# Kernel tuning notes

Hardware: AMD Instinct MI355X
Metric: run time of the kernel (lower is better)

## Reference

```python
import jax, jax.numpy as jnp
import numpy as np

HIDDEN = 2048
N_HEADS = 16
HEAD_DIM = HIDDEN // N_HEADS
ROPE_BASE = 10000.0


def rotate_half(x):
    half = x.shape[-1] // 2
    return jnp.concatenate((-x[..., half:], x[..., :half]), axis=-1)


def rope_cos_sin(seq_len, dtype):
    inv_freq = 1.0 / (ROPE_BASE ** (jnp.arange(0, HEAD_DIM, 2, dtype=jnp.float32) / HEAD_DIM))
    pos = jnp.arange(seq_len, dtype=jnp.float32)
    freqs = jnp.einsum('i,j->ij', pos, inv_freq)  # [S, hd/2]
    emb = jnp.concatenate((freqs, freqs), axis=-1)  # [S, hd]
    return jnp.cos(emb).astype(dtype), jnp.sin(emb).astype(dtype)


def setup_inputs() -> dict:
    key = jax.random.key(0)
    ks = jax.random.split(key, 9)
    B, S, H = 2, 2048, HIDDEN
    std = 1.0 / np.sqrt(H)
    return {
        'hidden_states': jax.random.normal(ks[0], (B, S, H), dtype=jnp.float32),
        'Wq': jax.random.uniform(ks[1], (H, H), jnp.float32, -std, std),
        'bq': jax.random.uniform(ks[2], (H,), jnp.float32, -std, std),
        'Wk': jax.random.uniform(ks[3], (H, H), jnp.float32, -std, std),
        'bk': jax.random.uniform(ks[4], (H,), jnp.float32, -std, std),
        'Wv': jax.random.uniform(ks[5], (H, H), jnp.float32, -std, std),
        'bv': jax.random.uniform(ks[6], (H,), jnp.float32, -std, std),
        'Wo': jax.random.uniform(ks[7], (H, H), jnp.float32, -std, std),
        'bo': jax.random.uniform(ks[8], (H,), jnp.float32, -std, std),
    }


def reference(hidden_states, Wq, bq, Wk, bk, Wv, bv, Wo, bo):
    B, S, H = hidden_states.shape
    scale = HEAD_DIM ** -0.5

    def proj(W, b):
        # torch Linear: x @ W.T + b
        y = jnp.einsum('bsh,oh->bso', hidden_states, W) + b
        return y.reshape(B, S, N_HEADS, HEAD_DIM).transpose(0, 2, 1, 3)  # [B,nh,S,hd]

    q = proj(Wq, bq)
    k = proj(Wk, bk)
    v = proj(Wv, bv)

    cos, sin = rope_cos_sin(S, hidden_states.dtype)  # [S, hd]
    cos = cos[None, None, :, :]
    sin = sin[None, None, :, :]
    q = q * cos + rotate_half(q) * sin
    k = k * cos + rotate_half(k) * sin

    scores = jnp.einsum('bhqd,bhkd->bhqk', q, k) * scale  # [B,nh,S,S]
    probs = jax.nn.softmax(scores, axis=-1)
    ctx = jnp.einsum('bhqk,bhkd->bhqd', probs, v)
    ctx = ctx.transpose(0, 2, 1, 3).reshape(B, S, H)
    return jnp.einsum('bsh,oh->bso', ctx, Wo) + bo
```

## Files before the change

kernel.cpp:

```cpp
#include <hip/hip_runtime.h>
#include <hip/hip_bf16.h>
#include <math.h>

#define HIDDEN 2048
#define NH 16
#define HD 128
#define NB 2
#define SEQ 2048
#define K_DIM 2048

typedef unsigned int u32;
typedef unsigned short ushort_t;
typedef __bf16 bf16x8 __attribute__((ext_vector_type(8)));
typedef float f32x4 __attribute__((ext_vector_type(4)));
typedef ushort_t u16x8 __attribute__((ext_vector_type(8)));

__device__ __forceinline__ void split1(float x, unsigned short& h, unsigned short& l) {
    u32 u = __float_as_uint(x);
    u32 hr = (u + 0x7FFFu + ((u >> 16) & 1u)) >> 16;
    h = (unsigned short)hr;
    float r = x - __uint_as_float(hr << 16);
    u32 u2 = __float_as_uint(r);
    l = (unsigned short)((u2 + 0x7FFFu + ((u2 >> 16) & 1u)) >> 16);
}

__device__ __forceinline__ ushort_t bf16r(float x) {
    u32 u = __float_as_uint(x);
    return (ushort_t)((u + 0x7FFFu + ((u >> 16) & 1u)) >> 16);
}

__device__ __forceinline__ void gl_lds16(const void* g, void* l) {
    __builtin_amdgcn_global_load_lds(
        (const __attribute__((address_space(1))) u32*)g,
        (__attribute__((address_space(3))) u32*)l, 16, 0, 0);
}

__global__ void k_rope_tables(float* __restrict__ ct, float* __restrict__ st) {
    int idx = blockIdx.x * 256 + threadIdx.x;
    int s = idx >> 6, d = idx & 63;
    double inv = pow(10000.0, -(double)d * (1.0 / 64.0));
    double ang = (double)s * inv;
    ct[idx] = (float)cos(ang);
    st[idx] = (float)sin(ang);
}

#define XG 2097152
#define WG 1048576
__global__ void k_cvt_all(const float4* __restrict__ X, const float4* __restrict__ W0,
                          const float4* __restrict__ W1, const float4* __restrict__ W2,
                          ushort4* __restrict__ Xh, ushort4* __restrict__ H0,
                          ushort4* __restrict__ H1, ushort4* __restrict__ H2) {
    int idx = blockIdx.x * 256 + threadIdx.x;
    const float4* src;
    ushort4* dst;
    int off;
    if (idx < XG) { src = X; dst = Xh; off = idx; }
    else {
        int t = idx - XG;
        int m = t >> 20;
        off = t & (WG - 1);
        src = (m == 0) ? W0 : (m == 1) ? W1 : W2;
        dst = (m == 0) ? H0 : (m == 1) ? H1 : H2;
    }
    float4 x = src[off];
    ushort4 h;
    h.x = bf16r(x.x); h.y = bf16r(x.y); h.z = bf16r(x.z); h.w = bf16r(x.w);
    dst[off] = h;
}

__global__ void k_split(const float4* __restrict__ src, ushort4* __restrict__ hi,
                        ushort4* __restrict__ lo) {
    int idx = blockIdx.x * 256 + threadIdx.x;
    float4 x = src[idx];
    ushort4 h, l;
    split1(x.x, h.x, l.x);
    split1(x.y, h.y, l.y);
    split1(x.z, h.z, l.z);
    split1(x.w, h.w, l.w);
    hi[idx] = h;
    lo[idx] = l;
}

__global__ __launch_bounds__(256)
void k_gemm_qkv(const ushort_t* __restrict__ Xh,
                const ushort_t* __restrict__ W0, const ushort_t* __restrict__ W1,
                const ushort_t* __restrict__ W2,
                const float* __restrict__ b0, const float* __restrict__ b1,
                const float* __restrict__ b2,
                float* __restrict__ o0, float* __restrict__ o1, float* __restrict__ o2) {
    __shared__ ushort_t As[128 * 32];
    __shared__ ushort_t Bs[128 * 32];
    const int tid = threadIdx.x;
    const int lane = tid & 63;
    const int w = tid >> 6;
    const int wm = w & 1, wn = w >> 1;
    const int quad = lane >> 4;
    const int l15 = lane & 15;
    const int m0 = blockIdx.x << 7;
    const int mat = blockIdx.y >> 4;
    const int n0 = (blockIdx.y & 15) << 7;
    const ushort_t* Wsel = (mat == 0) ? W0 : (mat == 1) ? W1 : W2;
    const float* bias = (mat == 0) ? b0 : (mat == 1) ? b1 : b2;
    float* out = (mat == 0) ? o0 : (mat == 1) ? o1 : o2;

    const ushort_t* src = (w < 2) ? Xh : Wsel;
    const int rbase = ((w < 2) ? m0 : n0) + (w & 1) * 64;
    ushort_t* lbase = ((w < 2) ? As : Bs) + (w & 1) * 64 * 32;
    const int lrow = lane >> 2;
    const int lk = (lane & 3) << 3;
    const ushort_t* gp[4];
    ushort_t* lp[4];
#pragma unroll
    for (int i = 0; i < 4; i++) {
        gp[i] = src + (size_t)(rbase + i * 16 + lrow) * K_DIM + lk;
        lp[i] = lbase + i * 512;
    }

    f32x4 acc[4][4];
#pragma unroll
    for (int i = 0; i < 4; i++)
#pragma unroll
        for (int j = 0; j < 4; j++) acc[i][j] = (f32x4){0.f, 0.f, 0.f, 0.f};

    const int aoff = (wm * 64 + l15) * 32 + quad * 8;
    const int boff = (wn * 64 + l15) * 32 + quad * 8;

#pragma unroll
    for (int i = 0; i < 4; i++) gl_lds16(gp[i], lp[i]);
    __syncthreads();
    bf16x8 ah[4], bh[4];
#pragma unroll
    for (int f = 0; f < 4; f++) {
        ah[f] = *(const bf16x8*)&As[aoff + f * 512];
        bh[f] = *(const bf16x8*)&Bs[boff + f * 512];
    }

    for (int kt = 32; kt <= K_DIM; kt += 32) {
        __syncthreads();
        if (kt < K_DIM) {
#pragma unroll
            for (int i = 0; i < 4; i++) gl_lds16(gp[i] + kt, lp[i]);
        }
#pragma unroll
        for (int fm = 0; fm < 4; fm++)
#pragma unroll
            for (int fn = 0; fn < 4; fn++)
                acc[fm][fn] = __builtin_amdgcn_mfma_f32_16x16x32_bf16(ah[fm], bh[fn], acc[fm][fn], 0, 0, 0);
        if (kt < K_DIM) {
            __syncthreads();
#pragma unroll
            for (int f = 0; f < 4; f++) {
                ah[f] = *(const bf16x8*)&As[aoff + f * 512];
                bh[f] = *(const bf16x8*)&Bs[boff + f * 512];
            }
        }
    }

    float bcolv[4];
#pragma unroll
    for (int fn = 0; fn < 4; fn++) bcolv[fn] = bias[n0 + wn * 64 + fn * 16 + l15];

    const int h = n0 >> 7;
    const int bb = m0 >> 11;
    const int sb = (m0 & (SEQ - 1)) + wm * 64 + quad * 4;
    const int d = wn * 64 + l15;
    float* obase = out + ((size_t)(bb * NH + h) * SEQ) * HD;
#pragma unroll
    for (int fm = 0; fm < 4; fm++)
#pragma unroll
        for (int fn = 0; fn < 4; fn++)
#pragma unroll
            for (int r = 0; r < 4; r++)
                obase[(size_t)(sb + fm * 16 + r) * HD + d + fn * 16] =
                    acc[fm][fn][r] + bcolv[fn];
}

__global__ __launch_bounds__(256)
void k_gemm_o(const ushort_t* __restrict__ Ah, const ushort_t* __restrict__ Al,
              const ushort_t* __restrict__ Bh, const ushort_t* __restrict__ Bl,
              const float* __restrict__ bias, float* __restrict__ out) {
    __shared__ ushort_t lds[4][128 * 32];
    const int tid = threadIdx.x;
    const int lane = tid & 63;
    const int w = tid >> 6;
    const int wm = w & 1, wn = w >> 1;
    const int quad = lane >> 4;
    const int l15 = lane & 15;
    const int m0 = blockIdx.x << 7;
    const int n0 = blockIdx.y << 7;
    const bool isA = (w < 2);

    const ushort_t* src = (w == 0) ? Ah : (w == 1) ? Al : (w == 2) ? Bh : Bl;
    const int lrow = lane >> 2;
    const int lk = (lane & 3) << 3;
    const ushort_t* gp[8];
    ushort_t* lp[8];
#pragma unroll
    for (int i = 0; i < 8; i++) {
        if (isA) {
            int m = m0 + i * 16 + lrow;
            int bb = m >> 11, s = m & (SEQ - 1);
            gp[i] = src + ((size_t)bb * NH * SEQ + s) * HD + lk;
        } else {
            gp[i] = src + (size_t)(n0 + i * 16 + lrow) * K_DIM + lk;
        }
        lp[i] = &lds[w][i * 512];
    }

    f32x4 acc[4][4];
#pragma unroll
    for (int i = 0; i < 4; i++)
#pragma unroll
        for (int j = 0; j < 4; j++) acc[i][j] = (f32x4){0.f, 0.f, 0.f, 0.f};

    const int aoff = (wm * 64 + l15) * 32 + quad * 8;
    const int boff = (wn * 64 + l15) * 32 + quad * 8;

#pragma unroll
    for (int i = 0; i < 8; i++) gl_lds16(gp[i], lp[i]);
    __syncthreads();
    bf16x8 ah[4], al[4], bh[4], bl[4];
#pragma unroll
    for (int f = 0; f < 4; f++) {
        ah[f] = *(const bf16x8*)&lds[0][aoff + f * 512];
        al[f] = *(const bf16x8*)&lds[1][aoff + f * 512];
        bh[f] = *(const bf16x8*)&lds[2][boff + f * 512];
        bl[f] = *(const bf16x8*)&lds[3][boff + f * 512];
    }

    for (int kt = 32; kt <= K_DIM; kt += 32) {
        __syncthreads();
        if (kt < K_DIM) {
            const size_t koff = isA ? ((size_t)(kt >> 7) * (SEQ * HD) + (kt & 127)) : (size_t)kt;
#pragma unroll
            for (int i = 0; i < 8; i++) gl_lds16(gp[i] + koff, lp[i]);
        }
#pragma unroll
        for (int fm = 0; fm < 4; fm++)
#pragma unroll
            for (int fn = 0; fn < 4; fn++) {
                acc[fm][fn] = __builtin_amdgcn_mfma_f32_16x16x32_bf16(ah[fm], bh[fn], acc[fm][fn], 0, 0, 0);
                acc[fm][fn] = __builtin_amdgcn_mfma_f32_16x16x32_bf16(ah[fm], bl[fn], acc[fm][fn], 0, 0, 0);
                acc[fm][fn] = __builtin_amdgcn_mfma_f32_16x16x32_bf16(al[fm], bh[fn], acc[fm][fn], 0, 0, 0);
            }
        if (kt < K_DIM) {
            __syncthreads();
#pragma unroll
            for (int f = 0; f < 4; f++) {
                ah[f] = *(const bf16x8*)&lds[0][aoff + f * 512];
                al[f] = *(const bf16x8*)&lds[1][aoff + f * 512];
                bh[f] = *(const bf16x8*)&lds[2][boff + f * 512];
                bl[f] = *(const bf16x8*)&lds[3][boff + f * 512];
            }
        }
    }

    float bcolv[4];
#pragma unroll
    for (int fn = 0; fn < 4; fn++) bcolv[fn] = bias[n0 + wn * 64 + fn * 16 + l15];

    const int mb = m0 + wm * 64 + quad * 4;
    const int nb = n0 + wn * 64 + l15;
#pragma unroll
    for (int fm = 0; fm < 4; fm++)
#pragma unroll
        for (int fn = 0; fn < 4; fn++)
#pragma unroll
            for (int r = 0; r < 4; r++)
                out[(size_t)(mb + fm * 16 + r) * HIDDEN + nb + fn * 16] =
                    acc[fm][fn][r] + bcolv[fn];
}

__global__ void k_rope_pack(const float* __restrict__ q, const float* __restrict__ k,
                            const float* __restrict__ ct, const float* __restrict__ st,
                            ushort_t* __restrict__ Qb, ushort_t* __restrict__ Kb) {
    int idx = blockIdx.x * 256 + threadIdx.x;
    int d = idx & 63;
    int s = (idx >> 6) & (SEQ - 1);
    int bh = idx >> 17;
    size_t base = ((size_t)bh * SEQ + s) * HD;
    float c = ct[(s << 6) + d], sn = st[(s << 6) + d];
    const float scq = 0.08838834764831845f;
    float q0 = q[base + d], q1 = q[base + d + 64];
    Qb[base + d]      = bf16r((q0 * c - q1 * sn) * scq);
    Qb[base + d + 64] = bf16r((q1 * c + q0 * sn) * scq);
    float k0 = k[base + d], k1 = k[base + d + 64];
    Kb[base + d]      = bf16r(k0 * c - k1 * sn);
    Kb[base + d + 64] = bf16r(k1 * c + k0 * sn);
}

__global__ __launch_bounds__(256)
void k_vpack(const float* __restrict__ v, ushort_t* __restrict__ vt) {
    __shared__ float t[64][65];
    const int tid = threadIdx.x;
    const int bh = blockIdx.z;
    const int s0 = blockIdx.x << 6;
    const int d0 = blockIdx.y << 6;
    const float* src = v + ((size_t)bh * SEQ + s0) * HD + d0;
    const int rr = tid >> 4;
    const int cc = (tid & 15) << 2;
#pragma unroll
    for (int i = 0; i < 4; i++) {
        float4 x = *(const float4*)(src + (size_t)(i * 16 + rr) * HD + cc);
        t[i * 16 + rr][cc] = x.x;
        t[i * 16 + rr][cc + 1] = x.y;
        t[i * 16 + rr][cc + 2] = x.z;
        t[i * 16 + rr][cc + 3] = x.w;
    }
    __syncthreads();
    const int dr = tid >> 2;
    const int sc_ = (tid & 3) << 4;
    ushort_t* dst = vt + ((size_t)bh * HD + d0 + dr) * SEQ + s0 + sc_;
    u16x8 o0, o1;
#pragma unroll
    for (int u = 0; u < 8; u++) o0[u] = bf16r(t[sc_ + u][dr]);
#pragma unroll
    for (int u = 0; u < 8; u++) o1[u] = bf16r(t[sc_ + 8 + u][dr]);
    *(u16x8*)dst = o0;
    *(u16x8*)(dst + 8) = o1;
}

__global__ __launch_bounds__(256, 2)
void k_flash_mfma(const ushort_t* __restrict__ Qb, const ushort_t* __restrict__ Kb,
                  const ushort_t* __restrict__ Vt,
                  ushort_t* __restrict__ ch, ushort_t* __restrict__ cl) {
    __shared__ ushort_t KV[128 * 136];
    __shared__ ushort_t Ps[128 * 136];
    const int tid = threadIdx.x;
    const int lane = tid & 63;
    const int w = tid >> 6;
    const int quad = lane >> 4;
    const int l15 = lane & 15;
    const int bi = blockIdx.x;
    const int bh = bi & 31;
    const int qt = bi >> 5;
    const ushort_t* Qg = Qb + ((size_t)bh * SEQ + ((size_t)qt << 7)) * HD;
    const ushort_t* Kg = Kb + (size_t)bh * SEQ * HD;
    const ushort_t* Vg = Vt + (size_t)bh * HD * SEQ;

    bf16x8 qf[2][4];
#pragma unroll
    for (int qi = 0; qi < 2; qi++)
#pragma unroll
        for (int ks = 0; ks < 4; ks++)
            qf[qi][ks] = *(const bf16x8*)(Qg + (size_t)(w * 32 + qi * 16 + l15) * HD + ks * 32 + quad * 8);

    const int sr = tid >> 4;
    const int sc8 = (tid & 15) << 3;

    u16x8 Kreg[8], Vreg[8];
#pragma unroll
    for (int i = 0; i < 8; i++)
        Kreg[i] = *(const u16x8*)(Kg + (size_t)(i * 16 + sr) * HD + sc8);
#pragma unroll
    for (int i = 0; i < 8; i++)
        Vreg[i] = *(const u16x8*)(Vg + (size_t)(i * 16 + sr) * SEQ + sc8);

    f32x4 acc[2][8];
#pragma unroll
    for (int qi = 0; qi < 2; qi++)
#pragma unroll
        for (int d = 0; d < 8; d++) acc[qi][d] = (f32x4){0.f, 0.f, 0.f, 0.f};
    float lp[2] = {0.f, 0.f};

    for (int kt = 0; kt < SEQ; kt += 128) {
        const int np = kt + 128;
        __syncthreads();
#pragma unroll
        for (int i = 0; i < 8; i++)
            *(u16x8*)&KV[(i * 16 + sr) * 136 + sc8] = Kreg[i];
        if (np < SEQ) {
#pragma unroll
            for (int i = 0; i < 8; i++)
                Kreg[i] = *(const u16x8*)(Kg + (size_t)(np + i * 16 + sr) * HD + sc8);
        }
        __syncthreads();

        f32x4 sc[2][8];
#pragma unroll
        for (int qi = 0; qi < 2; qi++)
#pragma unroll
            for (int j = 0; j < 8; j++) sc[qi][j] = (f32x4){0.f, 0.f, 0.f, 0.f};
#pragma unroll
        for (int ks = 0; ks < 4; ks++) {
#pragma unroll
            for (int jh = 0; jh < 2; jh++) {
                bf16x8 kf[4];
#pragma unroll
                for (int j = 0; j < 4; j++)
                    kf[j] = *(const bf16x8*)&KV[((jh * 4 + j) * 16 + l15) * 136 + ks * 32 + quad * 8];
#pragma unroll
                for (int qi = 0; qi < 2; qi++)
#pragma unroll
                    for (int j = 0; j < 4; j++)
                        sc[qi][jh * 4 + j] = __builtin_amdgcn_mfma_f32_16x16x32_bf16(
                            kf[j], qf[qi][ks], sc[qi][jh * 4 + j], 0, 0, 0);
            }
        }

#pragma unroll
        for (int qi = 0; qi < 2; qi++) {
            const int prow = (w * 32 + qi * 16 + l15) * 136 + quad * 4;
#pragma unroll
            for (int j = 0; j < 8; j++) {
                float p0 = __expf(sc[qi][j][0]);
                float p1 = __expf(sc[qi][j][1]);
                float p2 = __expf(sc[qi][j][2]);
                float p3 = __expf(sc[qi][j][3]);
                lp[qi] += (p0 + p1) + (p2 + p3);
                __hip_bfloat162 lo2 = __float22bfloat162_rn({p0, p1});
                __hip_bfloat162 hi2 = __float22bfloat162_rn({p2, p3});
                uint2 pk = make_uint2(*(u32*)&lo2, *(u32*)&hi2);
                *(uint2*)&Ps[prow + j * 16] = pk;
            }
        }
        __syncthreads();
#pragma unroll
        for (int i = 0; i < 8; i++)
            *(u16x8*)&KV[(i * 16 + sr) * 136 + sc8] = Vreg[i];
        if (np < SEQ) {
#pragma unroll
            for (int i = 0; i < 8; i++)
                Vreg[i] = *(const u16x8*)(Vg + (size_t)(i * 16 + sr) * SEQ + np + sc8);
        }
        __syncthreads();

#pragma unroll
        for (int ks = 0; ks < 4; ks++) {
            bf16x8 pf[2];
#pragma unroll
            for (int qi = 0; qi < 2; qi++)
                pf[qi] = *(const bf16x8*)&Ps[(w * 32 + qi * 16 + l15) * 136 + ks * 32 + quad * 8];
#pragma unroll
            for (int db = 0; db < 8; db++) {
                bf16x8 vf = *(const bf16x8*)&KV[(db * 16 + l15) * 136 + ks * 32 + quad * 8];
#pragma unroll
                for (int qi = 0; qi < 2; qi++)
                    acc[qi][db] = __builtin_amdgcn_mfma_f32_16x16x32_bf16(vf, pf[qi], acc[qi][db], 0, 0, 0);
            }
        }
    }

    float inv[2];
#pragma unroll
    for (int qi = 0; qi < 2; qi++) {
        float l = lp[qi];
        l += __shfl_xor(l, 16);
        l += __shfl_xor(l, 32);
        inv[qi] = 1.0f / l;
    }
    const size_t obase = ((size_t)bh * SEQ + ((size_t)qt << 7)) * HD;

    __syncthreads();
#pragma unroll
    for (int qi = 0; qi < 2; qi++)
#pragma unroll
        for (int db = 0; db < 8; db++) {
            ushort4 hh;
            ushort_t dum;
            split1(acc[qi][db][0] * inv[qi], hh.x, dum);
            split1(acc[qi][db][1] * inv[qi], hh.y, dum);
            split1(acc[qi][db][2] * inv[qi], hh.z, dum);
            split1(acc[qi][db][3] * inv[qi], hh.w, dum);
            *(ushort4*)&Ps[(w * 32 + qi * 16 + l15) * 136 + db * 16 + quad * 4] = hh;
        }
    __syncthreads();
#pragma unroll
    for (int t = 0; t < 8; t++) {
        int c = t * 256 + tid;
        int row = c >> 4, col8 = (c & 15) << 3;
        *(u16x8*)&ch[obase + (size_t)row * HD + col8] = *(const u16x8*)&Ps[row * 136 + col8];
    }
    __syncthreads();
#pragma unroll
    for (int qi = 0; qi < 2; qi++)
#pragma unroll
        for (int db = 0; db < 8; db++) {
            ushort4 ll;
            ushort_t dum;
            split1(acc[qi][db][0] * inv[qi], dum, ll.x);
            split1(acc[qi][db][1] * inv[qi], dum, ll.y);
            split1(acc[qi][db][2] * inv[qi], dum, ll.z);
            split1(acc[qi][db][3] * inv[qi], dum, ll.w);
            *(ushort4*)&Ps[(w * 32 + qi * 16 + l15) * 136 + db * 16 + quad * 4] = ll;
        }
    __syncthreads();
#pragma unroll
    for (int t = 0; t < 8; t++) {
        int c = t * 256 + tid;
        int row = c >> 4, col8 = (c & 15) << 3;
        *(u16x8*)&cl[obase + (size_t)row * HD + col8] = *(const u16x8*)&Ps[row * 136 + col8];
    }
}

extern "C" void kernel_launch(void* const* d_in, const int* in_sizes, int n_in,
                              void* d_out, int out_size, void* d_ws, size_t ws_size,
                              hipStream_t stream) {
    const float* X  = (const float*)d_in[0];
    const float* Wq = (const float*)d_in[1];
    const float* bq = (const float*)d_in[2];
    const float* Wk = (const float*)d_in[3];
    const float* bk = (const float*)d_in[4];
    const float* Wv = (const float*)d_in[5];
    const float* bv = (const float*)d_in[6];
    const float* Wo = (const float*)d_in[7];
    const float* bo = (const float*)d_in[8];
    float* out = (float*)d_out;

    const size_t QS = (size_t)NB * NH * SEQ * HD;
    const size_t WS = (size_t)HIDDEN * HIDDEN;
    float* q_ws = (float*)d_ws;
    float* k_ws = q_ws + QS;
    float* v_ws = k_ws + QS;
    float* cost = v_ws + QS;
    float* sint = cost + (size_t)SEQ * 64;
    ushort_t* Xh = (ushort_t*)(sint + (size_t)SEQ * 64);
    ushort_t* Wh0 = Xh + QS;
    ushort_t* Wh1 = Wh0 + WS;
    ushort_t* Wh2 = Wh1 + WS;
    ushort_t* Woh = Wh2 + WS;
    ushort_t* Wol = Woh + WS;
    ushort_t* Kb  = Wol + WS;
    ushort_t* Vtb = Kb + QS;
    ushort_t* ctxh = (ushort_t*)q_ws;
    ushort_t* ctxl = ctxh + QS;

    k_rope_tables<<<(SEQ * 64) / 256, 256, 0, stream>>>(cost, sint);

    k_cvt_all<<<(XG + 3 * WG) / 256, 256, 0, stream>>>(
        (const float4*)X, (const float4*)Wq, (const float4*)Wk, (const float4*)Wv,
        (ushort4*)Xh, (ushort4*)Wh0, (ushort4*)Wh1, (ushort4*)Wh2);
    k_split<<<WS / 4 / 256, 256, 0, stream>>>((const float4*)Wo, (ushort4*)Woh, (ushort4*)Wol);

    k_gemm_qkv<<<dim3(32, 48), 256, 0, stream>>>(Xh, Wh0, Wh1, Wh2, bq, bk, bv,
                                                 q_ws, k_ws, v_ws);

    ushort_t* Qbb = Xh;
    k_rope_pack<<<(NB * NH * SEQ * 64) / 256, 256, 0, stream>>>(q_ws, k_ws, cost, sint, Qbb, Kb);
    k_vpack<<<dim3(SEQ / 64, HD / 64, NB * NH), 256, 0, stream>>>(v_ws, Vtb);

    k_flash_mfma<<<512, 256, 0, stream>>>(Qbb, Kb, Vtb, ctxh, ctxl);

    k_gemm_o<<<dim3(32, 16), 256, 0, stream>>>(ctxh, ctxl, Woh, Wol, bo, out);
}
```

Before: 500.8 us.

## Rewrite QKV GEMM as 256x256-tile 8-wave kernel with double-buffered swizzled LDS

Replaces the 128x128, 4-wave QKV projection GEMM with a 256x256-tile, 512-thread kernel that uses a K-step of 64 and double-buffered LDS. The main loop is interleaved into phases so global-to-LDS loads overlap MFMA work, with explicit waitcnt, barriers and s_setprio. LDS columns are XOR-swizzled to reduce bank conflicts, and block IDs are remapped for better L2 locality. The larger tile raises data reuse per block, at the cost of only 384 blocks and heavy register and LDS use (128 KB), which may limit occupancy.

```diff
diff --git a/kernel.cpp b/kernel.cpp
--- a/kernel.cpp
+++ b/kernel.cpp
@@ -81,98 +81,158 @@
     lo[idx] = l;
 }
 
-__global__ __launch_bounds__(256)
-void k_gemm_qkv(const ushort_t* __restrict__ Xh,
-                const ushort_t* __restrict__ W0, const ushort_t* __restrict__ W1,
-                const ushort_t* __restrict__ W2,
-                const float* __restrict__ b0, const float* __restrict__ b1,
-                const float* __restrict__ b2,
-                float* __restrict__ o0, float* __restrict__ o1, float* __restrict__ o2) {
-    __shared__ ushort_t As[128 * 32];
-    __shared__ ushort_t Bs[128 * 32];
+#define BAR  __builtin_amdgcn_s_barrier()
+#define LGKM0 asm volatile("s_waitcnt lgkmcnt(0)" ::: "memory")
+#define VM4  asm volatile("s_waitcnt vmcnt(4)" ::: "memory")
+#define VM0  asm volatile("s_waitcnt vmcnt(0)" ::: "memory")
+#define PRIO1 __builtin_amdgcn_s_setprio(1)
+#define PRIO0 __builtin_amdgcn_s_setprio(0)
+
+#define STA(slot, half, kt) do { \
+    const ushort_t* g_ = Xh + sgA + (size_t)((half) * 128) * 2048 + (size_t)(kt) * 64; \
+    gl_lds16(g_, &As[slot][((half) * 128 + w * 16) * 64]); \
+    gl_lds16(g_ + 8 * 2048, &As[slot][((half) * 128 + w * 16 + 8) * 64]); \
+} while (0)
+
+#define STB(slot, half, kt) do { \
+    const ushort_t* g_ = Wsel + sgB + (size_t)((half) * 128) * 2048 + (size_t)(kt) * 64; \
+    gl_lds16(g_, &Bs[slot][((half) * 128 + w * 16) * 64]); \
+    gl_lds16(g_ + 8 * 2048, &Bs[slot][((half) * 128 + w * 16 + 8) * 64]); \
+} while (0)
+
+#define RD_A4(DST, slot, MB) \
+    _Pragma("unroll") for (int mf = 0; mf < 4; mf++) { \
+        DST[mf][0] = *(const bf16x8*)&As[slot][arow + ((MB) + mf) * 1024 + cc0]; \
+        DST[mf][1] = *(const bf16x8*)&As[slot][arow + ((MB) + mf) * 1024 + cc1]; \
+    }
+
+#define RD_B2(DST, slot, NBB) \
+    _Pragma("unroll") for (int nf = 0; nf < 2; nf++) { \
+        DST[nf][0] = *(const bf16x8*)&Bs[slot][brow + ((NBB) + nf) * 1024 + cc0]; \
+        DST[nf][1] = *(const bf16x8*)&Bs[slot][brow + ((NBB) + nf) * 1024 + cc1]; \
+    }
+
+#define PH_MFMA(AF, BF, MB, NBB) do { PRIO1; \
+    _Pragma("unroll") for (int mf = 0; mf < 4; mf++) \
+    _Pragma("unroll") for (int nf = 0; nf < 2; nf++) { \
+        acc[(MB) + mf][(NBB) + nf] = __builtin_amdgcn_mfma_f32_16x16x32_bf16( \
+            AF[mf][0], BF[nf][0], acc[(MB) + mf][(NBB) + nf], 0, 0, 0); \
+        acc[(MB) + mf][(NBB) + nf] = __builtin_amdgcn_mfma_f32_16x16x32_bf16( \
+            AF[mf][1], BF[nf][1], acc[(MB) + mf][(NBB) + nf], 0, 0, 0); \
+    } PRIO0; } while (0)
+
+__global__ __launch_bounds__(512, 2)
+void k_gemm_qkv8(const ushort_t* __restrict__ Xh,
+                 const ushort_t* __restrict__ W0, const ushort_t* __restrict__ W1,
+                 const ushort_t* __restrict__ W2,
+                 const float* __restrict__ b0, const float* __restrict__ b1,
+                 const float* __restrict__ b2,
+                 float* __restrict__ o0, float* __restrict__ o1, float* __restrict__ o2) {
+    __shared__ ushort_t As[2][256 * 64];
+    __shared__ ushort_t Bs[2][256 * 64];
     const int tid = threadIdx.x;
     const int lane = tid & 63;
     const int w = tid >> 6;
-    const int wm = w & 1, wn = w >> 1;
+    const int wm = w >> 2;
+    const int wn = w & 3;
     const int quad = lane >> 4;
     const int l15 = lane & 15;
-    const int m0 = blockIdx.x << 7;
-    const int mat = blockIdx.y >> 4;
-    const int n0 = (blockIdx.y & 15) << 7;
+
+    int bid = blockIdx.x;
+    bid = (bid & 7) * 48 + (bid >> 3);
+    const int bx = bid & 15;
+    const int by = bid >> 4;
+    const int m0 = bx << 8;
+    const int mat = by >> 3;
+    const int n0 = (by & 7) << 8;
     const ushort_t* Wsel = (mat == 0) ? W0 : (mat == 1) ? W1 : W2;
     const float* bias = (mat == 0) ? b0 : (mat == 1) ? b1 : b2;
     float* out = (mat == 0) ? o0 : (mat == 1) ? o1 : o2;
 
-    const ushort_t* src = (w < 2) ? Xh : Wsel;
-    const int rbase = ((w < 2) ? m0 : n0) + (w & 1) * 64;
-    ushort_t* lbase = ((w < 2) ? As : Bs) + (w & 1) * 64 * 32;
-    const int lrow = lane >> 2;
-    const int lk = (lane & 3) << 3;
-    const ushort_t* gp[4];
-    ushort_t* lp[4];
-#pragma unroll
-    for (int i = 0; i < 4; i++) {
-        gp[i] = src + (size_t)(rbase + i * 16 + lrow) * K_DIM + lk;
-        lp[i] = lbase + i * 512;
-    }
-
-    f32x4 acc[4][4];
-#pragma unroll
-    for (int i = 0; i < 4; i++)
+    const int lrow = lane >> 3;
+    const int lcol8 = (((lane & 7) ^ lrow) << 3);
+    const size_t sgA = (size_t)(m0 + w * 16 + lrow) * 2048 + lcol8;
+    const size_t sgB = (size_t)(n0 + w * 16 + lrow) * 2048 + lcol8;
+
+    const int arow = (wm * 128 + l15) * 64;
+    const int brow = (wn * 64 + l15) * 64;
+    const int cc0 = ((quad ^ (l15 & 7)) << 3);
+    const int cc1 = cc0 ^ 32;
+
+    f32x4 acc[8][4];
+#pragma unroll
+    for (int i = 0; i < 8; i++)
 #pragma unroll
         for (int j = 0; j < 4; j++) acc[i][j] = (f32x4){0.f, 0.f, 0.f, 0.f};
 
-    const int aoff = (wm * 64 + l15) * 32 + quad * 8;
-    const int boff = (wn * 64 + l15) * 32 + quad * 8;
-
-#pragma unroll
-    for (int i = 0; i < 4; i++) gl_lds16(gp[i], lp[i]);
-    __syncthreads();
-    bf16x8 ah[4], bh[4];
-#pragma unroll
-    for (int f = 0; f < 4; f++) {
-        ah[f] = *(const bf16x8*)&As[aoff + f * 512];
-        bh[f] = *(const bf16x8*)&Bs[boff + f * 512];
-    }
-
-    for (int kt = 32; kt <= K_DIM; kt += 32) {
-        __syncthreads();
-        if (kt < K_DIM) {
-#pragma unroll
-            for (int i = 0; i < 4; i++) gl_lds16(gp[i] + kt, lp[i]);
-        }
-#pragma unroll
-        for (int fm = 0; fm < 4; fm++)
-#pragma unroll
-            for (int fn = 0; fn < 4; fn++)
-                acc[fm][fn] = __builtin_amdgcn_mfma_f32_16x16x32_bf16(ah[fm], bh[fn], acc[fm][fn], 0, 0, 0);
-        if (kt < K_DIM) {
-            __syncthreads();
-#pragma unroll
-            for (int f = 0; f < 4; f++) {
-                ah[f] = *(const bf16x8*)&As[aoff + f * 512];
-                bh[f] = *(const bf16x8*)&Bs[boff + f * 512];
+    STA(0, 0, 0); STA(0, 1, 0);
+    STB(0, 0, 0); STB(0, 1, 0);
+    STA(1, 0, 1); STA(1, 1, 1);
+
+    bf16x8 a03[4][2], a47[4][2], b01[2][2], b23[2][2];
+
+    for (int it = 0; it < 16; ++it) {
+        const int kt0 = 2 * it, kt1 = 2 * it + 1;
+        const bool st = (it < 15);
+        VM4; BAR;
+        RD_A4(a03, 0, 0); RD_B2(b01, 0, 0);
+        STB(1, 0, kt1);
+        BAR; LGKM0;
+        PH_MFMA(a03, b01, 0, 0);
+        BAR;
+        RD_A4(a47, 0, 4); RD_B2(b23, 0, 2);
+        STB(1, 1, kt1);
+        BAR; LGKM0;
+        PH_MFMA(a03, b23, 0, 2);
+        BAR;
+        if (st) STA(0, 0, kt0 + 2);
+        BAR;
+        PH_MFMA(a47, b01, 4, 0);
+        BAR;
+        if (st) STA(0, 1, kt0 + 2);
+        BAR;
+        PH_MFMA(a47, b23, 4, 2);
+        if (it == 15) { VM0; } else { VM4; }
+        BAR;
+        RD_A4(a03, 1, 0); RD_B2(b01, 1, 0);
+        if (st) STB(0, 0, kt0 + 2);
+        BAR; LGKM0;
+        PH_MFMA(a03, b01, 0, 0);
+        BAR;
+        RD_A4(a47, 1, 4); RD_B2(b23, 1, 2);
+        if (st) STB(0, 1, kt0 + 2);
+        BAR; LGKM0;
+        PH_MFMA(a03, b23, 0, 2);
+        BAR;
+        if (st) STA(1, 0, kt1 + 2);
+        BAR;
+        PH_MFMA(a47, b01, 4, 0);
+        BAR;
+        if (st) STA(1, 1, kt1 + 2);
+        BAR;
+        PH_MFMA(a47, b23, 4, 2);
+    }
+
+    float bcolv[4];
+#pragma unroll
+    for (int nf = 0; nf < 4; nf++) bcolv[nf] = bias[n0 + wn * 64 + nf * 16 + l15];
+
+    const int mbase = m0 + wm * 128 + quad * 4;
+#pragma unroll
+    for (int mf = 0; mf < 8; mf++)
+#pragma unroll
+        for (int nf = 0; nf < 4; nf++) {
+            const int n = n0 + wn * 64 + nf * 16 + l15;
+            const int hh = n >> 7;
+            const int d = n & 127;
+#pragma unroll
+            for (int r = 0; r < 4; r++) {
+                const int m = mbase + mf * 16 + r;
+                const int bb = m >> 11;
+                const int s = m & (SEQ - 1);
+                out[((size_t)(bb * NH + hh) * SEQ + s) * HD + d] = acc[mf][nf][r] + bcolv[nf];
             }
         }
-    }
-
-    float bcolv[4];
-#pragma unroll
-    for (int fn = 0; fn < 4; fn++) bcolv[fn] = bias[n0 + wn * 64 + fn * 16 + l15];
-
-    const int h = n0 >> 7;
-    const int bb = m0 >> 11;
-    const int sb = (m0 & (SEQ - 1)) + wm * 64 + quad * 4;
-    const int d = wn * 64 + l15;
-    float* obase = out + ((size_t)(bb * NH + h) * SEQ) * HD;
-#pragma unroll
-    for (int fm = 0; fm < 4; fm++)
-#pragma unroll
-        for (int fn = 0; fn < 4; fn++)
-#pragma unroll
-            for (int r = 0; r < 4; r++)
-                obase[(size_t)(sb + fm * 16 + r) * HD + d + fn * 16] =
-                    acc[fm][fn][r] + bcolv[fn];
 }
 
 __global__ __launch_bounds__(256)
@@ -532,8 +592,8 @@
         (ushort4*)Xh, (ushort4*)Wh0, (ushort4*)Wh1, (ushort4*)Wh2);
     k_split<<<WS / 4 / 256, 256, 0, stream>>>((const float4*)Wo, (ushort4*)Woh, (ushort4*)Wol);
 
-    k_gemm_qkv<<<dim3(32, 48), 256, 0, stream>>>(Xh, Wh0, Wh1, Wh2, bq, bk, bv,
-                                                 q_ws, k_ws, v_ws);
+    k_gemm_qkv8<<<384, 512, 0, stream>>>(Xh, Wh0, Wh1, Wh2, bq, bk, bv,
+                                         q_ws, k_ws, v_ws);
 
     ushort_t* Qbb = Xh;
     k_rope_pack<<<(NB * NH * SEQ * 64) / 256, 256, 0, stream>>>(q_ws, k_ws, cost, sint, Qbb, Kb);
```

Result: no change. 504.4 us (+0.7%).
